# Kernel optimization log

Hardware: AMD Instinct MI355X
Metric: run time of the kernel (lower is better)

Reference implementation:

```python
import jax, jax.numpy as jnp
import numpy as np

N = 50000
E = 800000
D = 128


def setup_inputs() -> dict:
    key = jax.random.key(0)
    ks = jax.random.split(key, 10)
    x = jax.random.normal(ks[0], (N, D), dtype=jnp.float32)
    edge_index = jax.random.randint(ks[1], (2, E), 0, N, dtype=jnp.int32)
    s = 1.0 / np.sqrt(D)
    W1 = jax.random.uniform(ks[2], (D, D), jnp.float32, -s, s)
    b1 = jnp.zeros((D,), jnp.float32)
    W2 = jax.random.uniform(ks[3], (D, D), jnp.float32, -s, s)
    b2 = jnp.zeros((D,), jnp.float32)
    Wt = jax.random.uniform(ks[4], (D, 1), jnp.float32, -s, s)
    bt = jnp.zeros((1,), jnp.float32)
    We = jax.random.uniform(ks[5], (D, 1), jnp.float32, -s, s)
    be = jnp.zeros((1,), jnp.float32)
    return {"x": x, "edge_index": edge_index, "W1": W1, "b1": b1,
            "W2": W2, "b2": b2, "Wt": Wt, "bt": bt, "We": We, "be": be}


def _gcn_norm(edge_index, n):
    # add self-loops, then symmetric normalization D^-1/2 (A+I) D^-1/2
    loop = jnp.arange(n, dtype=edge_index.dtype)
    src = jnp.concatenate([edge_index[0], loop])
    dst = jnp.concatenate([edge_index[1], loop])
    ones = jnp.ones(src.shape[0], dtype=jnp.float32)
    deg = jax.ops.segment_sum(ones, dst, num_segments=n)
    dinv = jnp.where(deg > 0, jax.lax.rsqrt(deg), 0.0)
    norm = dinv[src] * dinv[dst]  # [E+N]
    return src, dst, norm


def _gcn_conv(h, W, b, src, dst, norm, n):
    h = h @ W                                   # [N, D'] dense GEMM
    msg = h[src] * norm[:, None]                # gather + scale
    out = jax.ops.segment_sum(msg, dst, num_segments=n)  # scatter-add
    return out + b


def reference(x, edge_index, W1, b1, W2, b2, Wt, bt, We, be):
    n = x.shape[0]
    src, dst, norm = _gcn_norm(edge_index, n)
    h = jax.nn.relu(_gcn_conv(x, W1, b1, src, dst, norm, n))
    h = jax.nn.relu(_gcn_conv(h, W2, b2, src, dst, norm, n))
    # dropout is identity at inference (eval mode)
    survival_time = h @ Wt + bt   # [N, 1]
    event_status = h @ We + be    # [N, 1]
    return survival_time, event_status
```

## Files before the change

### kernel.cpp

```cpp
#include <hip/hip_runtime.h>
#include <hip/hip_fp16.h>
#include <math.h>

#define NN 50000
#define NE 800000
#define DD 128

#define NB  196
#define CAP 5300
#define EPB 4096
#define A_BLOCKS 196

#define CONV_B 6250

#define SLAB2 (NN * 64)

typedef _Float16 half8_t __attribute__((ext_vector_type(8)));
typedef float f32x4 __attribute__((ext_vector_type(4)));


__global__ __launch_bounds__(256) void k_setup(const int* __restrict__ src, const int* __restrict__ dst,
                                               int* __restrict__ bcnt, int* __restrict__ deg,
                                               unsigned int* __restrict__ ebuf,
                                               const float* __restrict__ x,
                                               const float* __restrict__ W1, const float* __restrict__ W2,
                                               __half* __restrict__ Xh,
                                               __half* __restrict__ WT1, __half* __restrict__ WT2) {
    const int blk = blockIdx.x;
    const int tid = threadIdx.x;

    if (blk < A_BLOCKS) {
        __shared__ int hist[256];
        __shared__ int scanbuf[256];
        __shared__ int gbase[256];
        __shared__ unsigned int stage[EPB];
        __shared__ int tgt[EPB];

        const int e0 = blk * EPB;
        int nE = NE - e0; if (nE > EPB) nE = EPB;

        hist[tid] = 0;
        __syncthreads();

        unsigned int pk[16];
        unsigned int br[16];
        #pragma unroll
        for (int j = 0; j < 16; ++j) {
            int idx = tid + j * 256;
            if (idx < nE) {
                int e = e0 + idx;
                int s = src[e], d = dst[e];
                int b = d >> 8;
                int r = atomicAdd(&hist[b], 1);
                atomicAdd(&deg[d], 1);
                pk[j] = (unsigned int)s | ((unsigned int)(d & 255) << 16);
                br[j] = (unsigned int)b | ((unsigned int)r << 8);
            }
        }
        __syncthreads();
        int v = hist[tid];
        scanbuf[tid] = v;
        __syncthreads();
        for (int o = 1; o < 256; o <<= 1) {
            int t2 = (tid >= o) ? scanbuf[tid - o] : 0;
            __syncthreads();
            scanbuf[tid] += t2;
            __syncthreads();
        }
        int base_excl = scanbuf[tid] - v;
        if (tid < NB && v > 0) gbase[tid] = tid * CAP + atomicAdd(&bcnt[tid], v);
        hist[tid] = base_excl;
        __syncthreads();

        #pragma unroll
        for (int j = 0; j < 16; ++j) {
            int idx = tid + j * 256;
            if (idx < nE) {
                int b = br[j] & 255;
                int r = (int)(br[j] >> 8);
                int pos = hist[b] + r;
                stage[pos] = pk[j];
                tgt[pos]   = gbase[b] + r;
            }
        }
        __syncthreads();
        #pragma unroll
        for (int j = 0; j < 16; ++j) {
            int idx = tid + j * 256;
            if (idx < nE) ebuf[tgt[idx]] = stage[idx];
        }
    } else if (blk < A_BLOCKS + CONV_B) {
        int idx = (blk - A_BLOCKS) * 256 + tid;
        if (idx < (NN * DD) / 4) {
            float4 v = ((const float4*)x)[idx];
            __half2 a = __floats2half2_rn(v.x, v.y);
            __half2 c = __floats2half2_rn(v.z, v.w);
            uint2 pk;
            pk.x = *(unsigned int*)&a;
            pk.y = *(unsigned int*)&c;
            int row = idx >> 5;
            int c16 = idx & 31;
            int ch = c16 >> 4, wi = c16 & 15;
            *(uint2*)(Xh + (size_t)ch * SLAB2 + (size_t)row * 64 + wi * 4) = pk;
        }
    } else {
        const float* W  = (blk == A_BLOCKS + CONV_B) ? W1 : W2;
        __half*      WT = (blk == A_BLOCKS + CONV_B) ? WT1 : WT2;
        int n = tid >> 1;
        int k0 = (tid & 1) * 64;
        #pragma unroll 8
        for (int j = 0; j < 64; ++j) {
            int k = k0 + j;
            WT[n * DD + k] = __float2half(W[k * DD + n]);
        }
    }
}


__global__ __launch_bounds__(256) void k_build_csr(const unsigned int* __restrict__ ebuf,
                                                   const int* __restrict__ bcnt,
                                                   const int* __restrict__ deg,
                                                   int* __restrict__ row_ptr,
                                                   float* __restrict__ dinv,
                                                   unsigned short* __restrict__ col) {
    __shared__ int cur[256];
    __shared__ int scanb[256];
    __shared__ unsigned short stage[CAP];

    const int b   = blockIdx.x;
    const int tid = threadIdx.x;
    const int seg0 = b * CAP;
    const int sb   = bcnt[b];
    const int n0   = b << 8;
    int nb = NN - n0; if (nb > 256) nb = 256;

    int sz_t = (tid < NB) ? bcnt[tid] : 0;
    scanb[tid] = sz_t;
    __syncthreads();
    for (int o = 1; o < 256; o <<= 1) {
        int t = (tid >= o) ? scanb[tid - o] : 0;
        __syncthreads();
        scanb[tid] += t;
        __syncthreads();
    }
    const int rbase = scanb[b] - sb;
    __syncthreads();

    int v = (tid < nb) ? deg[n0 + tid] : 0;
    scanb[tid] = v;
    __syncthreads();
    for (int o = 1; o < 256; o <<= 1) {
        int t = (tid >= o) ? scanb[tid - o] : 0;
        __syncthreads();
        scanb[tid] += t;
        __syncthreads();
    }
    int excl = scanb[tid] - v;
    if (tid < nb) {
        row_ptr[n0 + tid] = rbase + excl;
        dinv[n0 + tid] = rsqrtf(1.0f + (float)v);
    }
    if (b == 0 && tid == 0) row_ptr[NN] = NE;
    cur[tid] = excl;
    __syncthreads();
    for (int p = tid; p < sb; p += 256) {
        unsigned int e = ebuf[seg0 + p];
        int pos = atomicAdd(&cur[(e >> 16) & 255], 1);
        stage[pos] = (unsigned short)(e & 0xFFFFu);
    }
    __syncthreads();
    for (int p = tid; p < sb; p += 256) {
        col[rbase + p] = stage[p];
    }
}


#define LPAD 136
#define GEMM_B 782
#define ZERO_B 98

__global__ __launch_bounds__(256) void k_gemm_mfma(const __half* __restrict__ Xc, const __half* __restrict__ WT,
                                                   const float* __restrict__ dinv, __half* __restrict__ Gc,
                                                   float* __restrict__ zbuf, int zcount) {
    const int tid = threadIdx.x;

    if (blockIdx.x >= GEMM_B) {
        int idx = (blockIdx.x - GEMM_B) * 256 + tid;
        if (idx * 4 + 3 < zcount) ((float4*)zbuf)[idx] = make_float4(0.f, 0.f, 0.f, 0.f);
        else {
            for (int k = idx * 4; k < zcount; ++k) zbuf[k] = 0.f;
        }
        return;
    }

    __shared__ __half Wl[DD * LPAD];
    __shared__ __half Al[64 * LPAD];

    const int row0 = blockIdx.x * 64;

    {
        const uint4* WTg = (const uint4*)WT;
        #pragma unroll
        for (int j = 0; j < 8; ++j) {
            int u = tid + j * 256;
            int n = u >> 4, koff = (u & 15) * 8;
            uint4 v = WTg[u];
            *(uint4*)&Wl[n * LPAD + koff] = v;
        }
    }
    {
        #pragma unroll
        for (int j = 0; j < 4; ++j) {
            int u = tid + j * 256;
            int r = u >> 4, c16 = u & 15;
            int ch = c16 >> 3, wi = c16 & 7;
            int grow = row0 + r;
            uint4 v;
            if (grow < NN) v = *(const uint4*)(Xc + (size_t)ch * SLAB2 + (size_t)grow * 64 + wi * 8);
            else { v.x = 0; v.y = 0; v.z = 0; v.w = 0; }
            *(uint4*)&Al[r * LPAD + c16 * 8] = v;
        }
    }
    __syncthreads();

    const int wave = tid >> 6;
    const int lane = tid & 63;
    const int m    = lane & 15;
    const int quad = lane >> 4;

    f32x4 acc[8];
    #pragma unroll
    for (int t = 0; t < 8; ++t) acc[t] = (f32x4){0.f, 0.f, 0.f, 0.f};

    #pragma unroll
    for (int kk = 0; kk < DD; kk += 32) {
        half8_t a = *(const half8_t*)&Al[(wave * 16 + m) * LPAD + kk + quad * 8];
        #pragma unroll
        for (int t = 0; t < 8; ++t) {
            half8_t b = *(const half8_t*)&Wl[(t * 16 + m) * LPAD + kk + quad * 8];
            acc[t] = __builtin_amdgcn_mfma_f32_16x16x32_f16(a, b, acc[t], 0, 0, 0);
        }
    }

    __syncthreads();

    float4 dv = *(const float4*)&dinv[row0 + wave * 16 + quad * 4];

    #pragma unroll
    for (int t = 0; t < 8; ++t) {
        #pragma unroll
        for (int r = 0; r < 4; ++r) {
            int row_l = wave * 16 + quad * 4 + r;
            int c     = t * 16 + m;
            float val = acc[t][r] * ((const float*)&dv)[r];
            Al[row_l * LPAD + c] = __float2half(val);
        }
    }
    __syncthreads();

    {
        #pragma unroll
        for (int j = 0; j < 4; ++j) {
            int u = tid + j * 256;
            int r = u >> 4, c16 = u & 15;
            int ch = c16 >> 3, wi = c16 & 7;
            int grow = row0 + r;
            if (grow < NN) {
                uint4 v = *(const uint4*)&Al[r * LPAD + c16 * 8];
                *(uint4*)(Gc + (size_t)ch * SLAB2 + (size_t)grow * 64 + wi * 8) = v;
            }
        }
    }
}


__device__ inline float4 h4_to_f4(uint2 r) {
    __half2 a = *(__half2*)&r.x;
    __half2 b = *(__half2*)&r.y;
    float2 lo = __half22float2(a), hi = __half22float2(b);
    return make_float4(lo.x, lo.y, hi.x, hi.y);
}

__device__ inline uint2 f4_to_h4(float4 v) {
    __half2 a = __floats2half2_rn(v.x, v.y);
    __half2 b = __floats2half2_rn(v.z, v.w);
    uint2 r;
    r.x = *(unsigned int*)&a;
    r.y = *(unsigned int*)&b;
    return r;
}

__device__ inline float4 gather_grp64(const __half* __restrict__ slab, int node, int fl,
                                      const unsigned short* __restrict__ col, int beg, int end) {
    const __half* base = slab + fl * 4;
    float4 accA = h4_to_f4(*(const uint2*)(base + (size_t)node * 64));
    float4 accB = make_float4(0.f, 0.f, 0.f, 0.f);
    int p = beg;
    for (; p + 3 < end; p += 4) {
        int s0 = col[p], s1 = col[p + 1], s2 = col[p + 2], s3 = col[p + 3];
        float4 v0 = h4_to_f4(*(const uint2*)(base + (size_t)s0 * 64));
        float4 v1 = h4_to_f4(*(const uint2*)(base + (size_t)s1 * 64));
        float4 v2 = h4_to_f4(*(const uint2*)(base + (size_t)s2 * 64));
        float4 v3 = h4_to_f4(*(const uint2*)(base + (size_t)s3 * 64));
        accA.x += v0.x + v1.x; accA.y += v0.y + v1.y; accA.z += v0.z + v1.z; accA.w += v0.w + v1.w;
        accB.x += v2.x + v3.x; accB.y += v2.y + v3.y; accB.z += v2.z + v3.z; accB.w += v2.w + v3.w;
    }
    for (; p < end; ++p) {
        int s0 = col[p];
        float4 v0 = h4_to_f4(*(const uint2*)(base + (size_t)s0 * 64));
        accA.x += v0.x; accA.y += v0.y; accA.z += v0.z; accA.w += v0.w;
    }
    accA.x += accB.x; accA.y += accB.y; accA.z += accB.z; accA.w += accB.w;
    return accA;
}

__global__ __launch_bounds__(256) void k_aggregate_c(const __half* __restrict__ G, const float* __restrict__ dinv,
                                                     const int* __restrict__ row_ptr, const unsigned short* __restrict__ col,
                                                     const float* __restrict__ bias, __half* __restrict__ H) {
    const int bx    = blockIdx.x;
    const int slot  = bx & 7;
    const int chunk = slot >> 2;
    const int nb    = (bx >> 3) * 4 + (slot & 3);
    const int g     = threadIdx.x >> 4;
    const int fl    = threadIdx.x & 15;
    const int node  = nb * 16 + g;
    if (node >= NN) return;

    const __half* slab = G + (size_t)chunk * SLAB2;
    int beg = row_ptr[node];
    int end = row_ptr[node + 1];
    float4 acc = gather_grp64(slab, node, fl, col, beg, end);

    float di = dinv[node];
    float4 bv = *(const float4*)(bias + chunk * 64 + fl * 4);
    float4 hv;
    hv.x = fmaxf(fmaf(di, acc.x, bv.x), 0.f);
    hv.y = fmaxf(fmaf(di, acc.y, bv.y), 0.f);
    hv.z = fmaxf(fmaf(di, acc.z, bv.z), 0.f);
    hv.w = fmaxf(fmaf(di, acc.w, bv.w), 0.f);
    *(uint2*)(H + (size_t)chunk * SLAB2 + (size_t)node * 64 + fl * 4) = f4_to_h4(hv);
}

__global__ __launch_bounds__(256) void k_aggregate_heads_c(const __half* __restrict__ G, const float* __restrict__ dinv,
                                                           const int* __restrict__ row_ptr, const unsigned short* __restrict__ col,
                                                           const float* __restrict__ bias,
                                                           const float* __restrict__ Wt, const float* __restrict__ bt,
                                                           const float* __restrict__ We, const float* __restrict__ be,
                                                           float* __restrict__ out) {
    const int bx    = blockIdx.x;
    const int slot  = bx & 7;
    const int chunk = slot >> 2;
    const int nb    = (bx >> 3) * 4 + (slot & 3);
    const int g     = threadIdx.x >> 4;
    const int fl    = threadIdx.x & 15;
    const int node  = nb * 16 + g;
    if (node >= NN) return;

    const __half* slab = G + (size_t)chunk * SLAB2;
    int beg = row_ptr[node];
    int end = row_ptr[node + 1];
    float4 acc = gather_grp64(slab, node, fl, col, beg, end);

    float di = dinv[node];
    float4 bv = *(const float4*)(bias + chunk * 64 + fl * 4);
    float hx = fmaxf(fmaf(di, acc.x, bv.x), 0.f);
    float hy = fmaxf(fmaf(di, acc.y, bv.y), 0.f);
    float hz = fmaxf(fmaf(di, acc.z, bv.z), 0.f);
    float hw = fmaxf(fmaf(di, acc.w, bv.w), 0.f);

    float4 wt = *(const float4*)(Wt + chunk * 64 + fl * 4);
    float4 we = *(const float4*)(We + chunk * 64 + fl * 4);
    float t  = hx * wt.x + hy * wt.y + hz * wt.z + hw * wt.w;
    float ev = hx * we.x + hy * we.y + hz * we.z + hw * we.w;
    #pragma unroll
    for (int o = 1; o < 16; o <<= 1) {
        t  += __shfl_xor(t, o, 64);
        ev += __shfl_xor(ev, o, 64);
    }
    if (fl == 0) {
        if (chunk == 0) { t += bt[0]; ev += be[0]; }
        atomicAdd(&out[node], t);
        atomicAdd(&out[NN + node], ev);
    }
}


extern "C" void kernel_launch(void* const* d_in, const int* in_sizes, int n_in,
                              void* d_out, int out_size, void* d_ws, size_t ws_size,
                              hipStream_t stream) {
    const float* x  = (const float*)d_in[0];
    const int*   ei = (const int*)d_in[1];
    const float* W1 = (const float*)d_in[2];
    const float* b1 = (const float*)d_in[3];
    const float* W2 = (const float*)d_in[4];
    const float* b2 = (const float*)d_in[5];
    const float* Wt = (const float*)d_in[6];
    const float* bt = (const float*)d_in[7];
    const float* We = (const float*)d_in[8];
    const float* be = (const float*)d_in[9];
    float* out = (float*)d_out;

    const int* srcI = ei;
    const int* dstI = ei + NE;

    char* w = (char*)d_ws;
    __half*         Xh    = (__half*)w;         w += (size_t)NN * DD * sizeof(__half);
    __half*         Gh    = (__half*)w;         w += (size_t)NN * DD * sizeof(__half);
    __half*         H1h   = (__half*)w;         w += (size_t)NN * DD * sizeof(__half);
    __half*         WT1   = (__half*)w;         w += (size_t)DD * DD * sizeof(__half);
    __half*         WT2   = (__half*)w;         w += (size_t)DD * DD * sizeof(__half);
    unsigned int*   ebuf  = (unsigned int*)w;   w += (size_t)NB * CAP * sizeof(unsigned int);
    unsigned short* col   = (unsigned short*)w; w += (size_t)NE * sizeof(unsigned short);
    float*          dinv  = (float*)w;          w += (size_t)(NN + 64) * sizeof(float);
    int*            rowp  = (int*)w;            w += (size_t)(NN + 1) * sizeof(int);
    int*            bcnt  = (int*)w;            w += (size_t)NB * sizeof(int);
    int*            deg   = (int*)w;            w += (size_t)NN * sizeof(int);

    const int SETUP_B = A_BLOCKS + CONV_B + 2;
    const int NBLK    = (NN + 15) / 16;
    const int AGG_B   = ((NBLK + 3) / 4) * 8;

    hipMemsetAsync(bcnt, 0, (size_t)(NB + NN) * sizeof(int), stream);

    hipLaunchKernelGGL(k_setup,     dim3(SETUP_B), dim3(256), 0, stream,
                       srcI, dstI, bcnt, deg, ebuf, x, W1, W2, Xh, WT1, WT2);
    hipLaunchKernelGGL(k_build_csr, dim3(NB),      dim3(256), 0, stream, ebuf, bcnt, deg, rowp, dinv, col);

    hipLaunchKernelGGL(k_gemm_mfma,   dim3(GEMM_B + ZERO_B), dim3(256), 0, stream, Xh, WT1, dinv, Gh, out, out_size);
    hipLaunchKernelGGL(k_aggregate_c, dim3(AGG_B),           dim3(256), 0, stream, Gh, dinv, rowp, col, b1, H1h);

    hipLaunchKernelGGL(k_gemm_mfma,         dim3(GEMM_B), dim3(256), 0, stream, H1h, WT2, dinv, Gh, out, 0);
    hipLaunchKernelGGL(k_aggregate_heads_c, dim3(AGG_B),  dim3(256), 0, stream, Gh, dinv, rowp, col, b2,
                       Wt, bt, We, be, out);
}
```

Baseline: 228.0 us.

## Fuse fp32-to-fp16 conversion into first GEMM and compute degrees in CSR build

The separate x-to-half conversion pass in the setup kernel is removed. A new first-layer GEMM kernel reads fp32 x directly and converts it to fp16 while staging it into LDS, which avoids writing and re-reading a half-precision copy of x. Per-node degrees are no longer counted with global atomics in setup; the CSR build kernel (now 512 threads) counts them with a shared-memory histogram over each bucket's edges. This drops the deg buffer and shrinks the memset, at the cost of an extra pass over ebuf in the CSR build.

```diff
diff --git a/kernel.cpp b/kernel.cpp
--- a/kernel.cpp
+++ b/kernel.cpp
@@ -11,8 +11,6 @@
 #define EPB 4096
 #define A_BLOCKS 196
 
-#define CONV_B 6250
-
 #define SLAB2 (NN * 64)
 
 typedef _Float16 half8_t __attribute__((ext_vector_type(8)));
@@ -20,11 +18,8 @@
 
 
 __global__ __launch_bounds__(256) void k_setup(const int* __restrict__ src, const int* __restrict__ dst,
-                                               int* __restrict__ bcnt, int* __restrict__ deg,
-                                               unsigned int* __restrict__ ebuf,
-                                               const float* __restrict__ x,
+                                               int* __restrict__ bcnt, unsigned int* __restrict__ ebuf,
                                                const float* __restrict__ W1, const float* __restrict__ W2,
-                                               __half* __restrict__ Xh,
                                                __half* __restrict__ WT1, __half* __restrict__ WT2) {
     const int blk = blockIdx.x;
     const int tid = threadIdx.x;
@@ -52,7 +47,6 @@
                 int s = src[e], d = dst[e];
                 int b = d >> 8;
                 int r = atomicAdd(&hist[b], 1);
-                atomicAdd(&deg[d], 1);
                 pk[j] = (unsigned int)s | ((unsigned int)(d & 255) << 16);
                 br[j] = (unsigned int)b | ((unsigned int)r << 8);
             }
@@ -89,23 +83,9 @@
             int idx = tid + j * 256;
             if (idx < nE) ebuf[tgt[idx]] = stage[idx];
         }
-    } else if (blk < A_BLOCKS + CONV_B) {
-        int idx = (blk - A_BLOCKS) * 256 + tid;
-        if (idx < (NN * DD) / 4) {
-            float4 v = ((const float4*)x)[idx];
-            __half2 a = __floats2half2_rn(v.x, v.y);
-            __half2 c = __floats2half2_rn(v.z, v.w);
-            uint2 pk;
-            pk.x = *(unsigned int*)&a;
-            pk.y = *(unsigned int*)&c;
-            int row = idx >> 5;
-            int c16 = idx & 31;
-            int ch = c16 >> 4, wi = c16 & 15;
-            *(uint2*)(Xh + (size_t)ch * SLAB2 + (size_t)row * 64 + wi * 4) = pk;
-        }
     } else {
-        const float* W  = (blk == A_BLOCKS + CONV_B) ? W1 : W2;
-        __half*      WT = (blk == A_BLOCKS + CONV_B) ? WT1 : WT2;
+        const float* W  = (blk == A_BLOCKS) ? W1 : W2;
+        __half*      WT = (blk == A_BLOCKS) ? WT1 : WT2;
         int n = tid >> 1;
         int k0 = (tid & 1) * 64;
         #pragma unroll 8
@@ -117,13 +97,12 @@
 }
 
 
-__global__ __launch_bounds__(256) void k_build_csr(const unsigned int* __restrict__ ebuf,
+__global__ __launch_bounds__(512) void k_build_csr(const unsigned int* __restrict__ ebuf,
                                                    const int* __restrict__ bcnt,
-                                                   const int* __restrict__ deg,
                                                    int* __restrict__ row_ptr,
                                                    float* __restrict__ dinv,
                                                    unsigned short* __restrict__ col) {
-    __shared__ int cur[256];
+    __shared__ int cnt[256];
     __shared__ int scanb[256];
     __shared__ unsigned short stage[CAP];
 
@@ -134,42 +113,50 @@
     const int n0   = b << 8;
     int nb = NN - n0; if (nb > 256) nb = 256;
 
-    int sz_t = (tid < NB) ? bcnt[tid] : 0;
-    scanb[tid] = sz_t;
+    if (tid < 256) scanb[tid] = (tid < NB) ? bcnt[tid] : 0;
     __syncthreads();
     for (int o = 1; o < 256; o <<= 1) {
-        int t = (tid >= o) ? scanb[tid - o] : 0;
-        __syncthreads();
-        scanb[tid] += t;
+        int t = 0;
+        if (tid < 256 && tid >= o) t = scanb[tid - o];
+        __syncthreads();
+        if (tid < 256) scanb[tid] += t;
         __syncthreads();
     }
     const int rbase = scanb[b] - sb;
     __syncthreads();
 
-    int v = (tid < nb) ? deg[n0 + tid] : 0;
-    scanb[tid] = v;
+    if (tid < 256) cnt[tid] = 0;
+    __syncthreads();
+    for (int p = tid; p < sb; p += 512) {
+        unsigned int e = ebuf[seg0 + p];
+        atomicAdd(&cnt[(e >> 16) & 255], 1);
+    }
+    __syncthreads();
+    int v = (tid < 256) ? cnt[tid] : 0;
+    if (tid < 256) scanb[tid] = v;
     __syncthreads();
     for (int o = 1; o < 256; o <<= 1) {
-        int t = (tid >= o) ? scanb[tid - o] : 0;
-        __syncthreads();
-        scanb[tid] += t;
-        __syncthreads();
-    }
-    int excl = scanb[tid] - v;
+        int t = 0;
+        if (tid < 256 && tid >= o) t = scanb[tid - o];
+        __syncthreads();
+        if (tid < 256) scanb[tid] += t;
+        __syncthreads();
+    }
+    int excl = (tid < 256) ? (scanb[tid] - v) : 0;
     if (tid < nb) {
         row_ptr[n0 + tid] = rbase + excl;
         dinv[n0 + tid] = rsqrtf(1.0f + (float)v);
     }
     if (b == 0 && tid == 0) row_ptr[NN] = NE;
-    cur[tid] = excl;
-    __syncthreads();
-    for (int p = tid; p < sb; p += 256) {
+    if (tid < 256) cnt[tid] = excl;
+    __syncthreads();
+    for (int p = tid; p < sb; p += 512) {
         unsigned int e = ebuf[seg0 + p];
-        int pos = atomicAdd(&cur[(e >> 16) & 255], 1);
+        int pos = atomicAdd(&cnt[(e >> 16) & 255], 1);
         stage[pos] = (unsigned short)(e & 0xFFFFu);
     }
     __syncthreads();
-    for (int p = tid; p < sb; p += 256) {
+    for (int p = tid; p < sb; p += 512) {
         col[rbase + p] = stage[p];
     }
 }
@@ -179,9 +166,9 @@
 #define GEMM_B 782
 #define ZERO_B 98
 
-__global__ __launch_bounds__(256) void k_gemm_mfma(const __half* __restrict__ Xc, const __half* __restrict__ WT,
-                                                   const float* __restrict__ dinv, __half* __restrict__ Gc,
-                                                   float* __restrict__ zbuf, int zcount) {
+__global__ __launch_bounds__(256) void k_gemm_x(const float* __restrict__ X, const __half* __restrict__ WT,
+                                                const float* __restrict__ dinv, __half* __restrict__ Gc,
+                                                float* __restrict__ zbuf, int zcount) {
     const int tid = threadIdx.x;
 
     if (blockIdx.x >= GEMM_B) {
@@ -196,6 +183,94 @@
     __shared__ __half Wl[DD * LPAD];
     __shared__ __half Al[64 * LPAD];
 
+    const int row0 = blockIdx.x * 64;
+
+    {
+        const uint4* WTg = (const uint4*)WT;
+        #pragma unroll
+        for (int j = 0; j < 8; ++j) {
+            int u = tid + j * 256;
+            int n = u >> 4, koff = (u & 15) * 8;
+            uint4 v = WTg[u];
+            *(uint4*)&Wl[n * LPAD + koff] = v;
+        }
+    }
+    {
+        const float4* X4 = (const float4*)X;
+        #pragma unroll
+        for (int j = 0; j < 8; ++j) {
+            int u = tid + j * 256;
+            int r = u >> 5, c4 = u & 31;
+            int grow = row0 + r;
+            float4 v = make_float4(0.f, 0.f, 0.f, 0.f);
+            if (grow < NN) v = X4[(size_t)grow * 32 + c4];
+            __half2 a = __floats2half2_rn(v.x, v.y);
+            __half2 b = __floats2half2_rn(v.z, v.w);
+            uint2 pk;
+            pk.x = *(unsigned int*)&a;
+            pk.y = *(unsigned int*)&b;
+            *(uint2*)&Al[r * LPAD + c4 * 4] = pk;
+        }
+    }
+    __syncthreads();
+
+    const int wave = tid >> 6;
+    const int lane = tid & 63;
+    const int m    = lane & 15;
+    const int quad = lane >> 4;
+
+    f32x4 acc[8];
+    #pragma unroll
+    for (int t = 0; t < 8; ++t) acc[t] = (f32x4){0.f, 0.f, 0.f, 0.f};
+
+    #pragma unroll
+    for (int kk = 0; kk < DD; kk += 32) {
+        half8_t a = *(const half8_t*)&Al[(wave * 16 + m) * LPAD + kk + quad * 8];
+        #pragma unroll
+        for (int t = 0; t < 8; ++t) {
+            half8_t b = *(const half8_t*)&Wl[(t * 16 + m) * LPAD + kk + quad * 8];
+            acc[t] = __builtin_amdgcn_mfma_f32_16x16x32_f16(a, b, acc[t], 0, 0, 0);
+        }
+    }
+
+    __syncthreads();
+
+    float4 dv = *(const float4*)&dinv[row0 + wave * 16 + quad * 4];
+
+    #pragma unroll
+    for (int t = 0; t < 8; ++t) {
+        #pragma unroll
+        for (int r = 0; r < 4; ++r) {
+            int row_l = wave * 16 + quad * 4 + r;
+            int c     = t * 16 + m;
+            float val = acc[t][r] * ((const float*)&dv)[r];
+            Al[row_l * LPAD + c] = __float2half(val);
+        }
+    }
+    __syncthreads();
+
+    {
+        #pragma unroll
+        for (int j = 0; j < 4; ++j) {
+            int u = tid + j * 256;
+            int r = u >> 4, c16 = u & 15;
+            int ch = c16 >> 3, wi = c16 & 7;
+            int grow = row0 + r;
+            if (grow < NN) {
+                uint4 v = *(const uint4*)&Al[r * LPAD + c16 * 8];
+                *(uint4*)(Gc + (size_t)ch * SLAB2 + (size_t)grow * 64 + wi * 8) = v;
+            }
+        }
+    }
+}
+
+
+__global__ __launch_bounds__(256) void k_gemm_h(const __half* __restrict__ Xc, const __half* __restrict__ WT,
+                                                const float* __restrict__ dinv, __half* __restrict__ Gc) {
+    __shared__ __half Wl[DD * LPAD];
+    __shared__ __half Al[64 * LPAD];
+
+    const int tid  = threadIdx.x;
     const int row0 = blockIdx.x * 64;
 
     {
@@ -404,7 +479,6 @@
     const int* dstI = ei + NE;
 
     char* w = (char*)d_ws;
-    __half*         Xh    = (__half*)w;         w += (size_t)NN * DD * sizeof(__half);
     __half*         Gh    = (__half*)w;         w += (size_t)NN * DD * sizeof(__half);
     __half*         H1h   = (__half*)w;         w += (size_t)NN * DD * sizeof(__half);
     __half*         WT1   = (__half*)w;         w += (size_t)DD * DD * sizeof(__half);
@@ -414,22 +488,21 @@
     float*          dinv  = (float*)w;          w += (size_t)(NN + 64) * sizeof(float);
     int*            rowp  = (int*)w;            w += (size_t)(NN + 1) * sizeof(int);
     int*            bcnt  = (int*)w;            w += (size_t)NB * sizeof(int);
-    int*            deg   = (int*)w;            w += (size_t)NN * sizeof(int);
-
-    const int SETUP_B = A_BLOCKS + CONV_B + 2;
+
+    const int SETUP_B = A_BLOCKS + 2;
     const int NBLK    = (NN + 15) / 16;
     const int AGG_B   = ((NBLK + 3) / 4) * 8;
 
-    hipMemsetAsync(bcnt, 0, (size_t)(NB + NN) * sizeof(int), stream);
+    hipMemsetAsync(bcnt, 0, (size_t)NB * sizeof(int), stream);
 
     hipLaunchKernelGGL(k_setup,     dim3(SETUP_B), dim3(256), 0, stream,
-                       srcI, dstI, bcnt, deg, ebuf, x, W1, W2, Xh, WT1, WT2);
-    hipLaunchKernelGGL(k_build_csr, dim3(NB),      dim3(256), 0, stream, ebuf, bcnt, deg, rowp, dinv, col);
-
-    hipLaunchKernelGGL(k_gemm_mfma,   dim3(GEMM_B + ZERO_B), dim3(256), 0, stream, Xh, WT1, dinv, Gh, out, out_size);
+                       srcI, dstI, bcnt, ebuf, W1, W2, WT1, WT2);
+    hipLaunchKernelGGL(k_build_csr, dim3(NB),      dim3(512), 0, stream, ebuf, bcnt, rowp, dinv, col);
+
+    hipLaunchKernelGGL(k_gemm_x,      dim3(GEMM_B + ZERO_B), dim3(256), 0, stream, x, WT1, dinv, Gh, out, out_size);
     hipLaunchKernelGGL(k_aggregate_c, dim3(AGG_B),           dim3(256), 0, stream, Gh, dinv, rowp, col, b1, H1h);
 
-    hipLaunchKernelGGL(k_gemm_mfma,         dim3(GEMM_B), dim3(256), 0, stream, H1h, WT2, dinv, Gh, out, 0);
+    hipLaunchKernelGGL(k_gemm_h,            dim3(GEMM_B), dim3(256), 0, stream, H1h, WT2, dinv, Gh);
     hipLaunchKernelGGL(k_aggregate_heads_c, dim3(AGG_B),  dim3(256), 0, stream, Gh, dinv, rowp, col, b2,
                        Wt, bt, We, be, out);
 }
```

New measurement: 201.6 us. 1.13x faster.
